# Performance work log

Hardware: AMD Instinct MI355X
Metric: run time of the kernel (lower is better)

The kernel has to match this reference:

```python
import jax, jax.numpy as jnp
import numpy as np

B, T, C = 2, 2048, 1024
H = 16
HS = C // H
EPS = 1e-5


def layernorm(x, g, b):
    mu = jnp.mean(x, axis=-1, keepdims=True)
    var = jnp.var(x, axis=-1, keepdims=True)
    return (x - mu) * jax.lax.rsqrt(var + EPS) * g + b


def setup_inputs() -> dict:
    key = jax.random.key(0)
    ks = jax.random.split(key, 12)
    s_in = 1.0 / np.sqrt(C)
    s_ff = 1.0 / np.sqrt(4 * C)
    return {
        "x": jax.random.normal(ks[0], (B, T, C), jnp.float32),
        "Wq": jax.random.normal(ks[1], (H, C, HS), jnp.float32) * s_in,
        "Wk": jax.random.normal(ks[2], (H, C, HS), jnp.float32) * s_in,
        "Wv": jax.random.normal(ks[3], (H, C, HS), jnp.float32) * s_in,
        "Wo": jax.random.normal(ks[4], (C, C), jnp.float32) * s_in,
        "bo": jnp.zeros((C,), jnp.float32),
        "W1": jax.random.normal(ks[5], (C, 4 * C), jnp.float32) * s_in,
        "b1": jnp.zeros((4 * C,), jnp.float32),
        "W2": jax.random.normal(ks[6], (4 * C, C), jnp.float32) * s_ff,
        "b2": jnp.zeros((C,), jnp.float32),
        "g1": jnp.ones((C,), jnp.float32),
        "be1": jnp.zeros((C,), jnp.float32),
        "g2": jnp.ones((C,), jnp.float32),
        "be2": jnp.zeros((C,), jnp.float32),
    }


def reference(x, Wq, Wk, Wv, Wo, bo, W1, b1, W2, b2, g1, be1, g2, be2):
    # x: [B,T,C]. Dropout is identity (eval mode).
    x = layernorm(x, g1, be1)
    # --- multi-head causal self-attention (per-source: scale by C**-0.5, NOT head_size) ---
    q = jnp.einsum("btc,hcd->bhtd", x, Wq)
    k = jnp.einsum("btc,hcd->bhtd", x, Wk)
    v = jnp.einsum("btc,hcd->bhtd", x, Wv)
    scores = jnp.einsum("bhtd,bhsd->bhts", q, k) * (C ** -0.5)  # [B,H,T,T]
    causal = jnp.tril(jnp.ones((T, T), bool))
    scores = jnp.where(causal, scores, -jnp.inf)
    wei = jax.nn.softmax(scores, axis=-1)
    attn = jnp.einsum("bhts,bhsd->bhtd", wei, v)
    attn = attn.transpose(0, 2, 1, 3).reshape(B, T, C)  # concat heads on last dim
    sa = attn @ Wo + bo
    x = x + sa
    # --- MLP with second pre-op LayerNorm ---
    x = layernorm(x, g2, be2)
    h = jax.nn.relu(x @ W1 + b1)
    x = x + (h @ W2 + b2)
    return x
```

## Files before the change

### kernel.cpp

```cpp
#include <hip/hip_runtime.h>
#include <hip/hip_bf16.h>
#include <math.h>

#define B_ 2
#define T_ 2048
#define C_ 1024
#define H_ 16
#define HS_ 64
#define N_ROWS (B_*T_)
#define MB (1024*1024)

typedef __attribute__((ext_vector_type(8))) short bf16x8;
typedef __attribute__((ext_vector_type(8))) unsigned short u16x8;
typedef __attribute__((ext_vector_type(4))) float floatx4;

static __device__ __forceinline__ unsigned short f2bf(float f) {
  union { float f; unsigned u; } v; v.f = f;
  unsigned r = v.u + 0x7fff + ((v.u >> 16) & 1);
  return (unsigned short)(r >> 16);
}
static __device__ __forceinline__ float bf2f(unsigned short s) {
  union { unsigned u; float f; } v; v.u = ((unsigned)s) << 16;
  return v.f;
}

__global__ __launch_bounds__(256) void ln_kernel(
    const float* __restrict__ x, const float* __restrict__ g,
    const float* __restrict__ b, unsigned short* __restrict__ outb)
{
  const int row = blockIdx.x;
  const int tid = threadIdx.x;
  const float* xr = x + (size_t)row * C_;
  float4 xv = *reinterpret_cast<const float4*>(xr + tid * 4);
  float s  = xv.x + xv.y + xv.z + xv.w;
  float ss = xv.x*xv.x + xv.y*xv.y + xv.z*xv.z + xv.w*xv.w;
  #pragma unroll
  for (int off = 32; off > 0; off >>= 1) {
    s  += __shfl_down(s, off, 64);
    ss += __shfl_down(ss, off, 64);
  }
  __shared__ float rs[4], rss[4];
  __shared__ float smu, srstd;
  if ((tid & 63) == 0) { rs[tid >> 6] = s; rss[tid >> 6] = ss; }
  __syncthreads();
  if (tid == 0) {
    float S  = rs[0] + rs[1] + rs[2] + rs[3];
    float SS = rss[0] + rss[1] + rss[2] + rss[3];
    float mu  = S * (1.0f / C_);
    float var = SS * (1.0f / C_) - mu * mu;
    smu = mu; srstd = rsqrtf(var + 1e-5f);
  }
  __syncthreads();
  const float mu = smu, rstd = srstd;
  float4 gv = *reinterpret_cast<const float4*>(g + tid * 4);
  float4 bv = *reinterpret_cast<const float4*>(b + tid * 4);
  union { unsigned long long ll; unsigned short s[4]; } o;
  o.s[0] = f2bf((xv.x - mu) * rstd * gv.x + bv.x);
  o.s[1] = f2bf((xv.y - mu) * rstd * gv.y + bv.y);
  o.s[2] = f2bf((xv.z - mu) * rstd * gv.z + bv.z);
  o.s[3] = f2bf((xv.w - mu) * rstd * gv.w + bv.w);
  *reinterpret_cast<unsigned long long*>(outb + (size_t)row * C_ + tid * 4) = o.ll;
}

__global__ __launch_bounds__(256) void transpose_cast(
    const float* __restrict__ in, unsigned short* __restrict__ out, int R, int Cc)
{
  __shared__ float tile[32][33];
  const int bz = blockIdx.z;
  in  += (size_t)bz * R * Cc;
  out += (size_t)bz * R * Cc;
  const int tx = threadIdx.x & 31;
  const int ty = threadIdx.x >> 5;
  const int c0 = blockIdx.x * 32, r0 = blockIdx.y * 32;
  #pragma unroll
  for (int j = 0; j < 4; ++j)
    tile[ty + j*8][tx] = in[(size_t)(r0 + ty + j*8) * Cc + c0 + tx];
  __syncthreads();
  #pragma unroll
  for (int j = 0; j < 4; ++j)
    out[(size_t)(c0 + ty + j*8) * R + r0 + tx] = f2bf(tile[tx][ty + j*8]);
}

__global__ __launch_bounds__(256) void transpose_cast_qkv(
    const float* __restrict__ Wq, const float* __restrict__ Wk,
    const float* __restrict__ Wv, unsigned short* __restrict__ out)
{
  __shared__ float tile[32][33];
  const int z = blockIdx.z;
  const int which = z >> 4, h = z & 15;
  const float* in = (which == 0 ? Wq : which == 1 ? Wk : Wv) + (size_t)h * C_ * HS_;
  unsigned short* dst = out + (size_t)z * C_ * HS_;
  const int tx = threadIdx.x & 31;
  const int ty = threadIdx.x >> 5;
  const int c0 = blockIdx.x * 32, r0 = blockIdx.y * 32;
  #pragma unroll
  for (int j = 0; j < 4; ++j)
    tile[ty + j*8][tx] = in[(size_t)(r0 + ty + j*8) * HS_ + c0 + tx];
  __syncthreads();
  #pragma unroll
  for (int j = 0; j < 4; ++j)
    dst[(size_t)(c0 + ty + j*8) * C_ + r0 + tx] = f2bf(tile[tx][ty + j*8]);
}

template<bool RELU, bool HASB>
__global__ __launch_bounds__(512, 2) void gemm256(
    const unsigned short* __restrict__ A,
    const unsigned short* __restrict__ Bt,
    const float* __restrict__ bias,
    unsigned short* __restrict__ Cout,
    int M, int N, int Kfull, int Kh)
{
  __shared__ __align__(16) unsigned short Asl[4 * 8192];
  __shared__ __align__(16) unsigned short Bsl[4 * 8192];
  const int tid = threadIdx.x;
  const int w = tid >> 6, l = tid & 63;
  const int wm = w & 1, wn = w >> 1;
  const int fr = l & 15, fq = l >> 4;
  const int m0 = blockIdx.x * 256, n0 = blockIdx.y * 256;
  const int z = blockIdx.z;

  const unsigned short* Aw = A  + (size_t)m0 * Kfull + (size_t)z * Kh;
  const unsigned short* Bw = Bt + (size_t)n0 * Kfull + (size_t)z * Kh;
  unsigned short* Cw = Cout + (size_t)z * M * N;

  const int g    = ((l & 3) - ((l >> 3) & 3)) & 3;
  const int srow = w * 16 + (l >> 2);
  const unsigned short* ga0 = Aw + (size_t)srow * Kfull + g * 8;
  const unsigned short* ga1 = ga0 + (size_t)128 * Kfull;
  const unsigned short* gb0 = Bw + (size_t)srow * Kfull + g * 8;
  const unsigned short* gb1 = gb0 + (size_t)128 * Kfull;
  unsigned short* da0 = Asl + w * 512;
  unsigned short* db0 = Bsl + w * 512;

  const int Qmax = (Kh >> 5) - 1;

  auto SA = [&](int q) {
    unsigned short* d = da0 + (q & 3) * 8192;
    __builtin_amdgcn_global_load_lds(
        (const __attribute__((address_space(1))) void*)(ga0 + q * 32),
        (__attribute__((address_space(3))) void*)d, 16, 0, 0);
    __builtin_amdgcn_global_load_lds(
        (const __attribute__((address_space(1))) void*)(ga1 + q * 32),
        (__attribute__((address_space(3))) void*)(d + 4096), 16, 0, 0);
  };
  auto SB = [&](int q) {
    unsigned short* d = db0 + (q & 3) * 8192;
    __builtin_amdgcn_global_load_lds(
        (const __attribute__((address_space(1))) void*)(gb0 + q * 32),
        (__attribute__((address_space(3))) void*)d, 16, 0, 0);
    __builtin_amdgcn_global_load_lds(
        (const __attribute__((address_space(1))) void*)(gb1 + q * 32),
        (__attribute__((address_space(3))) void*)(d + 4096), 16, 0, 0);
  };

  const int slot8 = ((fq + (fr >> 1)) & 3) * 8;
  const int aoff = (wm * 128 + fr) * 32 + slot8;
  const int boff = (wn * 64  + fr) * 32 + slot8;

  floatx4 acc[8][4] = {};

  SA(0); SB(0);
  if (Qmax >= 1) { SA(1); SB(1); }
  if (Qmax >= 2) { SA(2); SB(2); }
  asm volatile("s_waitcnt vmcnt(8)" ::: "memory");
  __builtin_amdgcn_s_barrier();

  #pragma unroll 1
  for (int q = 0; q <= Qmax; ++q) {
    const unsigned short* Ar = Asl + (q & 3) * 8192;
    const unsigned short* Br = Bsl + (q & 3) * 8192;
    const bool st = (q + 3 <= Qmax);

    bf16x8 af[4], bfr[4];
    #pragma unroll
    for (int mf = 0; mf < 4; ++mf)
      af[mf] = *(const bf16x8*)(Ar + aoff + mf * 512);
    #pragma unroll
    for (int nf = 0; nf < 4; ++nf)
      bfr[nf] = *(const bf16x8*)(Br + boff + nf * 512);
    if (st) SA(q + 3);
    __builtin_amdgcn_s_barrier();
    asm volatile("s_waitcnt lgkmcnt(0)" ::: "memory");
    __builtin_amdgcn_s_setprio(1);
    #pragma unroll
    for (int mf = 0; mf < 4; ++mf)
      #pragma unroll
      for (int nf = 0; nf < 4; ++nf)
        acc[mf][nf] = __builtin_amdgcn_mfma_f32_16x16x32_bf16(
            af[mf], bfr[nf], acc[mf][nf], 0, 0, 0);
    __builtin_amdgcn_s_setprio(0);
    __builtin_amdgcn_s_barrier();

    bf16x8 af2[4];
    #pragma unroll
    for (int mf = 0; mf < 4; ++mf)
      af2[mf] = *(const bf16x8*)(Ar + aoff + (4 + mf) * 512);
    if (st) SB(q + 3);
    if (q + 3 <= Qmax)        { asm volatile("s_waitcnt vmcnt(8)" ::: "memory"); }
    else if (q + 2 == Qmax)   { asm volatile("s_waitcnt vmcnt(4)" ::: "memory"); }
    else if (q + 1 == Qmax)   { asm volatile("s_waitcnt vmcnt(0)" ::: "memory"); }
    __builtin_amdgcn_s_barrier();
    asm volatile("s_waitcnt lgkmcnt(0)" ::: "memory");
    __builtin_amdgcn_s_setprio(1);
    #pragma unroll
    for (int mf = 0; mf < 4; ++mf)
      #pragma unroll
      for (int nf = 0; nf < 4; ++nf)
        acc[4 + mf][nf] = __builtin_amdgcn_mfma_f32_16x16x32_bf16(
            af2[mf], bfr[nf], acc[4 + mf][nf], 0, 0, 0);
    __builtin_amdgcn_s_setprio(0);
    __builtin_amdgcn_s_barrier();
  }

  #pragma unroll
  for (int nf = 0; nf < 4; ++nf) {
    const int col = n0 + wn * 64 + nf * 16 + fr;
    const float bv = HASB ? bias[col] : 0.0f;
    #pragma unroll
    for (int mf = 0; mf < 8; ++mf) {
      #pragma unroll
      for (int r = 0; r < 4; ++r) {
        const int row = m0 + wm * 128 + mf * 16 + fq * 4 + r;
        float v = acc[mf][nf][r] + bv;
        if (RELU) v = v > 0.0f ? v : 0.0f;
        Cw[(size_t)row * N + col] = f2bf(v);
      }
    }
  }
}

template<int TNB, bool OUTBF16, bool RELU, bool HASB, bool HASRES>
__global__ __launch_bounds__(256) void gemm_bf16(
    const unsigned short* __restrict__ A,
    const unsigned short* __restrict__ Bt,
    const float* __restrict__ bias,
    const unsigned short* __restrict__ res,
    void* __restrict__ Cout,
    int M, int N, int K)
{
  constexpr int NT = TNB / 32;
  constexpr int WN = TNB / 2;
  constexpr int LOADS = 4 + 2 * (TNB / 64);
  __shared__ unsigned short As[2][2][128 * 32];
  __shared__ unsigned short Bs[2][2][TNB * 32];
  const int tid  = threadIdx.x;
  const int lane = tid & 63;
  const int wave = tid >> 6;
  const int wm = wave & 1, wn = wave >> 1;
  const int m0 = blockIdx.x * 128, n0 = blockIdx.y * TNB;

  const int lrow = lane >> 2;
  const int lcol = (lane & 3) * 8;
  const int fr = lane & 15;
  const int fq = lane >> 4;

  floatx4 acc[4][NT] = {};

  const unsigned short* Aw = A  + (size_t)m0 * K;
  const unsigned short* Bw = Bt + (size_t)n0 * K;

  auto STAGE = [&](int bb, int k0) {
    #pragma unroll
    for (int half = 0; half < 2; ++half) {
      #pragma unroll
      for (int i = 0; i < 2; ++i) {
        const int rbase = i * 64 + wave * 16;
        const unsigned short* gp =
            Aw + (size_t)(rbase + lrow) * K + k0 + half * 32 + lcol;
        __builtin_amdgcn_global_load_lds(
            (const __attribute__((address_space(1))) void*)gp,
            (__attribute__((address_space(3))) void*)(As[bb][half] + rbase * 32),
            16, 0, 0);
      }
      #pragma unroll
      for (int i = 0; i < TNB / 64; ++i) {
        const int rbase = i * 64 + wave * 16;
        const unsigned short* gp =
            Bw + (size_t)(rbase + lrow) * K + k0 + half * 32 + lcol;
        __builtin_amdgcn_global_load_lds(
            (const __attribute__((address_space(1))) void*)gp,
            (__attribute__((address_space(3))) void*)(Bs[bb][half] + rbase * 32),
            16, 0, 0);
      }
    }
  };

  auto COMPUTE = [&](int bb) {
    #pragma unroll
    for (int half = 0; half < 2; ++half) {
      bf16x8 af[4], bfr[NT];
      #pragma unroll
      for (int t = 0; t < 4; ++t)
        af[t]  = *reinterpret_cast<const bf16x8*>(
            As[bb][half] + (wm*64 + t*16 + fr)*32 + fq*8);
      #pragma unroll
      for (int t = 0; t < NT; ++t)
        bfr[t] = *reinterpret_cast<const bf16x8*>(
            Bs[bb][half] + (wn*WN + t*16 + fr)*32 + fq*8);
      #pragma unroll
      for (int mt = 0; mt < 4; ++mt)
        #pragma unroll
        for (int nt = 0; nt < NT; ++nt)
          acc[mt][nt] = __builtin_amdgcn_mfma_f32_16x16x32_bf16(
              af[mt], bfr[nt], acc[mt][nt], 0, 0, 0);
    }
  };

  STAGE(0, 0);
  int bb = 0;
  for (int k0 = 64; k0 < K; k0 += 64) {
    STAGE(bb ^ 1, k0);
    asm volatile("s_waitcnt vmcnt(%0)" :: "n"(LOADS) : "memory");
    __builtin_amdgcn_s_barrier();
    COMPUTE(bb);
    __builtin_amdgcn_s_barrier();
    bb ^= 1;
  }
  asm volatile("s_waitcnt vmcnt(0)" ::: "memory");
  __builtin_amdgcn_s_barrier();
  COMPUTE(bb);

  #pragma unroll
  for (int nt = 0; nt < NT; ++nt) {
    const int col = n0 + wn*WN + nt*16 + fr;
    const float bv = HASB ? bias[col] : 0.0f;
    #pragma unroll
    for (int mt = 0; mt < 4; ++mt) {
      #pragma unroll
      for (int r = 0; r < 4; ++r) {
        const int row = m0 + wm*64 + mt*16 + fq*4 + r;
        float v = acc[mt][nt][r] + bv;
        if (RELU) v = v > 0.0f ? v : 0.0f;
        if (HASRES) v += bf2f(res[(size_t)row * N + col]);
        if (OUTBF16) ((unsigned short*)Cout)[(size_t)row * N + col] = f2bf(v);
        else         ((float*)Cout)[(size_t)row * N + col] = v;
      }
    }
  }
}

template<int SPLITS>
__global__ __launch_bounds__(256) void splitk_reduce(
    const unsigned short* __restrict__ p,
    const float* __restrict__ bias, const unsigned short* __restrict__ res,
    float* __restrict__ out)
{
  const size_t i = ((size_t)blockIdx.x * 256 + threadIdx.x) * 4;
  const size_t MN = (size_t)N_ROWS * C_;
  float4 bv = *reinterpret_cast<const float4*>(bias + (i & (size_t)(C_ - 1)));
  float acc[4] = {bv.x, bv.y, bv.z, bv.w};
  {
    const unsigned short* rp = res + i;
    #pragma unroll
    for (int j = 0; j < 4; ++j) acc[j] += bf2f(rp[j]);
  }
  #pragma unroll
  for (int z = 0; z < SPLITS; ++z) {
    const unsigned short* pp = p + (size_t)z * MN + i;
    #pragma unroll
    for (int j = 0; j < 4; ++j) acc[j] += bf2f(pp[j]);
  }
  float4 o; o.x = acc[0]; o.y = acc[1]; o.z = acc[2]; o.w = acc[3];
  *reinterpret_cast<float4*>(out + i) = o;
}

__global__ __launch_bounds__(256) void v_transpose(
    const unsigned short* __restrict__ qkv, unsigned short* __restrict__ vt)
{
  __shared__ __align__(16) unsigned short sT[64][72];
  const int st = blockIdx.x;
  const int bh = blockIdx.y;
  const int b = bh >> 4, h = bh & 15;
  const int t = threadIdx.x;
  const int r = t >> 2, c0 = (t & 3) * 16;
  const unsigned short* src =
      qkv + (size_t)(b * T_ + st * 64 + r) * 3072 + 2048 + h * 64 + c0;
  *(u16x8*)&sT[r][c0]     = *(const u16x8*)src;
  *(u16x8*)&sT[r][c0 + 8] = *(const u16x8*)(src + 8);
  __syncthreads();
  const int d = t >> 2, sc = (t & 3) * 16;
  unsigned short v[16];
  #pragma unroll
  for (int j = 0; j < 16; ++j) v[j] = sT[sc + j][d];
  unsigned short* dst = vt + ((size_t)bh * 64 + d) * (size_t)T_ + st * 64 + sc;
  *(uint4*)dst       = *(uint4*)&v[0];
  *(uint4*)(dst + 8) = *(uint4*)&v[8];
}

__global__ __launch_bounds__(256, 3) void attn_mfma(
    const unsigned short* __restrict__ qkv,
    const unsigned short* __restrict__ vt,
    unsigned short* __restrict__ out)
{
  const int bh = blockIdx.x;
  const int qt = (int)(gridDim.y - 1) - (int)blockIdx.y;
  const int b = bh >> 4, h = bh & 15;
  const int tid = threadIdx.x;
  const int w = tid >> 6;
  const int lane = tid & 63;
  const int l15 = lane & 15, fq = lane >> 4;
  const int t0 = qt * 64;
  const int q_row = t0 + w * 16 + l15;

  __shared__ __align__(16) unsigned short sK [128][72];
  __shared__ __align__(16) unsigned short sVt[64][136];
  __shared__ __align__(16) unsigned short sP [64][136];

  const float c1 = 1.4426950408889634f / 32.0f;

  bf16x8 aq[2];
  {
    const unsigned short* qp = qkv + (size_t)(b*T_ + q_row)*3072 + h*HS_ + fq*8;
    aq[0] = *(const bf16x8*)qp;
    aq[1] = *(const bf16x8*)(qp + 32);
  }

  const int nks = (qt >> 1) + 1;

  const int kr = tid >> 1, kc = (tid & 1) * 32;
  const int vr = tid >> 2, vc = (tid & 3) * 32;
  const unsigned short* kp0 =
      qkv + (size_t)(b*T_ + kr)*3072 + C_ + h*HS_ + kc;
  const unsigned short* vp0 =
      vt + ((size_t)bh*64 + vr)*(size_t)T_ + vc;

  u16x8 kg0, kg1, kg2, kg3, vg0, vg1, vg2, vg3;
  kg0 = *(const u16x8*)kp0;      kg1 = *(const u16x8*)(kp0 + 8);
  kg2 = *(const u16x8*)(kp0+16); kg3 = *(const u16x8*)(kp0 + 24);
  vg0 = *(const u16x8*)vp0;      vg1 = *(const u16x8*)(vp0 + 8);
  vg2 = *(const u16x8*)(vp0+16); vg3 = *(const u16x8*)(vp0 + 24);
  *(u16x8*)&sK [kr][kc]      = kg0; *(u16x8*)&sK [kr][kc + 8]  = kg1;
  *(u16x8*)&sK [kr][kc + 16] = kg2; *(u16x8*)&sK [kr][kc + 24] = kg3;
  *(u16x8*)&sVt[vr][vc]      = vg0; *(u16x8*)&sVt[vr][vc + 8]  = vg1;
  *(u16x8*)&sVt[vr][vc + 16] = vg2; *(u16x8*)&sVt[vr][vc + 24] = vg3;

  floatx4 oacc[4] = {};
  float m_s = -3.0e38f, l_s = 0.0f;

  #pragma unroll 1
  for (int ks = 0; ks < nks; ++ks) {
    asm volatile("s_waitcnt lgkmcnt(0)" ::: "memory");
    __builtin_amdgcn_s_barrier();

    if (ks + 1 < nks) {
      const unsigned short* kp = kp0 + (size_t)(ks + 1) * (128 * 3072);
      kg0 = *(const u16x8*)kp;        kg1 = *(const u16x8*)(kp + 8);
      kg2 = *(const u16x8*)(kp + 16); kg3 = *(const u16x8*)(kp + 24);
      const unsigned short* vp = vp0 + (ks + 1) * 128;
      vg0 = *(const u16x8*)vp;        vg1 = *(const u16x8*)(vp + 8);
      vg2 = *(const u16x8*)(vp + 16); vg3 = *(const u16x8*)(vp + 24);
    }

    floatx4 stacc[8] = {};
    __builtin_amdgcn_s_setprio(1);
    #pragma unroll
    for (int st = 0; st < 8; ++st) {
      bf16x8 ka = *(const bf16x8*)&sK[st*16 + l15][fq*8];
      bf16x8 kb = *(const bf16x8*)&sK[st*16 + l15][32 + fq*8];
      stacc[st] = __builtin_amdgcn_mfma_f32_16x16x32_bf16(ka, aq[0], stacc[st], 0, 0, 0);
      stacc[st] = __builtin_amdgcn_mfma_f32_16x16x32_bf16(kb, aq[1], stacc[st], 0, 0, 0);
    }
    __builtin_amdgcn_s_setprio(0);

    if (ks == nks - 1) {
      const int sbase = ks*128 + fq*4;
      #pragma unroll
      for (int st = 0; st < 8; ++st)
        #pragma unroll
        for (int r = 0; r < 4; ++r)
          if (sbase + st*16 + r > q_row) stacc[st][r] = -3.0e38f;
    }

    float mx = -3.0e38f;
    #pragma unroll
    for (int st = 0; st < 8; ++st)
      #pragma unroll
      for (int r = 0; r < 4; ++r) mx = fmaxf(mx, stacc[st][r]);
    mx = fmaxf(mx, __shfl_xor(mx, 16, 64));
    mx = fmaxf(mx, __shfl_xor(mx, 32, 64));

    float mnew;
    if (__all((mx - m_s) * c1 <= 8.0f)) {
      mnew = m_s;
    } else {
      mnew = fmaxf(m_s, mx);
      const float alpha = __builtin_amdgcn_exp2f((m_s - mnew) * c1);
      #pragma unroll
      for (int r = 0; r < 4; ++r) {
        const float ar = __shfl(alpha, fq*4 + r, 64);
        #pragma unroll
        for (int dt = 0; dt < 4; ++dt) oacc[dt][r] *= ar;
      }
      l_s *= alpha;
      m_s = mnew;
    }

    const float mc = mnew * c1;
    float sum = 0.0f;
    #pragma unroll
    for (int st = 0; st < 8; ++st) {
      unsigned pu[4];
      #pragma unroll
      for (int r = 0; r < 4; ++r) {
        const float p = __builtin_amdgcn_exp2f(stacc[st][r] * c1 - mc);
        sum += p;
        union { float f; unsigned u; } cv; cv.f = p;
        pu[r] = cv.u + 0x8000u;
      }
      const unsigned lo = __builtin_amdgcn_perm(pu[1], pu[0], 0x07060302u);
      const unsigned hi = __builtin_amdgcn_perm(pu[3], pu[2], 0x07060302u);
      *(unsigned long long*)&sP[w*16 + l15][st*16 + fq*4] =
          ((unsigned long long)hi << 32) | lo;
    }
    sum += __shfl_xor(sum, 16, 64);
    sum += __shfl_xor(sum, 32, 64);
    l_s += sum;

    __builtin_amdgcn_s_setprio(1);
    #pragma unroll
    for (int c = 0; c < 4; ++c) {
      bf16x8 ap = *(const bf16x8*)&sP[w*16 + l15][c*32 + fq*8];
      #pragma unroll
      for (int dt = 0; dt < 4; ++dt) {
        bf16x8 bv = *(const bf16x8*)&sVt[dt*16 + l15][c*32 + fq*8];
        oacc[dt] = __builtin_amdgcn_mfma_f32_16x16x32_bf16(ap, bv, oacc[dt], 0, 0, 0);
      }
    }
    __builtin_amdgcn_s_setprio(0);

    asm volatile("s_waitcnt lgkmcnt(0)" ::: "memory");
    __builtin_amdgcn_s_barrier();
    if (ks + 1 < nks) {
      *(u16x8*)&sK [kr][kc]      = kg0; *(u16x8*)&sK [kr][kc + 8]  = kg1;
      *(u16x8*)&sK [kr][kc + 16] = kg2; *(u16x8*)&sK [kr][kc + 24] = kg3;
      *(u16x8*)&sVt[vr][vc]      = vg0; *(u16x8*)&sVt[vr][vc + 8]  = vg1;
      *(u16x8*)&sVt[vr][vc + 16] = vg2; *(u16x8*)&sVt[vr][vc + 24] = vg3;
    }
  }

  #pragma unroll
  for (int r = 0; r < 4; ++r) {
    const float il = 1.0f / __shfl(l_s, fq*4 + r, 64);
    const int q = t0 + w*16 + fq*4 + r;
    #pragma unroll
    for (int dt = 0; dt < 4; ++dt)
      out[(size_t)(b*T_ + q)*C_ + h*HS_ + dt*16 + l15] = f2bf(oacc[dt][r] * il);
  }
}

extern "C" void kernel_launch(void* const* d_in, const int* in_sizes, int n_in,
                              void* d_out, int out_size, void* d_ws, size_t ws_size,
                              hipStream_t stream)
{
  const float* x   = (const float*)d_in[0];
  const float* Wq  = (const float*)d_in[1];
  const float* Wk  = (const float*)d_in[2];
  const float* Wv  = (const float*)d_in[3];
  const float* Wo  = (const float*)d_in[4];
  const float* bo  = (const float*)d_in[5];
  const float* W1  = (const float*)d_in[6];
  const float* b1  = (const float*)d_in[7];
  const float* W2  = (const float*)d_in[8];
  const float* b2  = (const float*)d_in[9];
  const float* g1  = (const float*)d_in[10];
  const float* be1 = (const float*)d_in[11];
  const float* g2  = (const float*)d_in[12];
  const float* be2 = (const float*)d_in[13];
  float* out = (float*)d_out;

  char* ws = (char*)d_ws;
  unsigned short* BtQKV = (unsigned short*)(ws + (size_t) 0*MB);
  unsigned short* BtWo  = (unsigned short*)(ws + (size_t) 6*MB);
  unsigned short* BtW1  = (unsigned short*)(ws + (size_t) 8*MB);
  unsigned short* BtW2  = (unsigned short*)(ws + (size_t)16*MB);
  unsigned short* lnb   = (unsigned short*)(ws + (size_t)24*MB);
  unsigned short* qkvb  = (unsigned short*)(ws + (size_t)32*MB);
  unsigned short* vtb   = (unsigned short*)(ws + (size_t)56*MB);
  unsigned short* attnb = (unsigned short*)(ws + (size_t)64*MB);
  float*          x2    = (float*)         (ws + (size_t)32*MB);
  unsigned short* hb    = (unsigned short*)(ws + (size_t)32*MB);
  unsigned short* pk4   = (unsigned short*)(ws + (size_t)64*MB);

  dim3 blk(256);
  dim3 blk512(512);

  transpose_cast_qkv<<<dim3(HS_/32, C_/32, 3*H_), blk, 0, stream>>>(Wq, Wk, Wv, BtQKV);
  transpose_cast<<<dim3(C_/32,  C_/32, 1),  blk, 0, stream>>>(Wo, BtWo, C_, C_);
  transpose_cast<<<dim3(4*C_/32,C_/32, 1),  blk, 0, stream>>>(W1, BtW1, C_, 4*C_);
  transpose_cast<<<dim3(C_/32,4*C_/32, 1),  blk, 0, stream>>>(W2, BtW2, 4*C_, C_);

  ln_kernel<<<dim3(N_ROWS), blk, 0, stream>>>(x, g1, be1, lnb);

  gemm256<false,false><<<dim3(N_ROWS/256, 3072/256, 1), blk512, 0, stream>>>(
      lnb, BtQKV, nullptr, qkvb, N_ROWS, 3072, C_, C_);

  v_transpose<<<dim3(T_/64, B_*H_), blk, 0, stream>>>(qkvb, vtb);

  attn_mfma<<<dim3(B_*H_, T_/64), blk, 0, stream>>>(qkvb, vtb, attnb);

  gemm_bf16<64,false,false,true,true><<<dim3(N_ROWS/128, C_/64), blk, 0, stream>>>(
      attnb, BtWo, bo, lnb, x2, N_ROWS, C_, C_);

  ln_kernel<<<dim3(N_ROWS), blk, 0, stream>>>(x2, g2, be2, lnb);

  gemm256<true,true><<<dim3(N_ROWS/256, 4*C_/256, 1), blk512, 0, stream>>>(
      lnb, BtW1, b1, hb, N_ROWS, 4*C_, C_, C_);

  gemm256<false,false><<<dim3(N_ROWS/256, C_/256, 4), blk512, 0, stream>>>(
      hb, BtW2, nullptr, pk4, N_ROWS, C_, 4*C_, C_);

  splitk_reduce<4><<<dim3((N_ROWS * C_) / (256 * 4)), blk, 0, stream>>>(
      pk4, b2, lnb, out);
}
```

Before: 342.9 us.

## Double-buffer GEMM LDS fragments and prefetch next k-step during MFMA

The GEMM main loop is restructured into a two-step unrolled HALF lambda. The next k-step's A and B fragments are read from LDS into a second register set (bfA/bfB ping-pong) while the second batch of MFMAs for the current step runs. Explicit lgkmcnt waits are dropped, and sched_barriers pin the instruction order. The aim is to hide LDS read latency behind matrix math, at the cost of more vector registers. The loop now assumes Qmax is odd.

```diff
diff --git a/kernel.cpp b/kernel.cpp
--- a/kernel.cpp
+++ b/kernel.cpp
@@ -158,58 +158,66 @@
   const int boff = (wn * 64  + fr) * 32 + slot8;
 
   floatx4 acc[8][4] = {};
+  bf16x8 af[4], af2[4], bfA[4], bfB[4];
 
   SA(0); SB(0);
   if (Qmax >= 1) { SA(1); SB(1); }
   if (Qmax >= 2) { SA(2); SB(2); }
   asm volatile("s_waitcnt vmcnt(8)" ::: "memory");
   __builtin_amdgcn_s_barrier();
-
-  #pragma unroll 1
-  for (int q = 0; q <= Qmax; ++q) {
-    const unsigned short* Ar = Asl + (q & 3) * 8192;
-    const unsigned short* Br = Bsl + (q & 3) * 8192;
-    const bool st = (q + 3 <= Qmax);
-
-    bf16x8 af[4], bfr[4];
+  #pragma unroll
+  for (int mf = 0; mf < 4; ++mf) af[mf]  = *(const bf16x8*)(Asl + aoff + mf * 512);
+  #pragma unroll
+  for (int nf = 0; nf < 4; ++nf) bfA[nf] = *(const bf16x8*)(Bsl + boff + nf * 512);
+
+  auto HALF = [&](int h, bf16x8 (&bfC)[4], bf16x8 (&bfN)[4]) {
+    const unsigned short* Ar = Asl + (h & 3) * 8192;
     #pragma unroll
     for (int mf = 0; mf < 4; ++mf)
-      af[mf] = *(const bf16x8*)(Ar + aoff + mf * 512);
-    #pragma unroll
-    for (int nf = 0; nf < 4; ++nf)
-      bfr[nf] = *(const bf16x8*)(Br + boff + nf * 512);
-    if (st) SA(q + 3);
-    __builtin_amdgcn_s_barrier();
-    asm volatile("s_waitcnt lgkmcnt(0)" ::: "memory");
+      af2[mf] = *(const bf16x8*)(Ar + aoff + (4 + mf) * 512);
+    if (h + 3 <= Qmax) SA(h + 3);
+    __builtin_amdgcn_sched_barrier(0);
+    __builtin_amdgcn_s_barrier();
     __builtin_amdgcn_s_setprio(1);
     #pragma unroll
     for (int mf = 0; mf < 4; ++mf)
       #pragma unroll
       for (int nf = 0; nf < 4; ++nf)
         acc[mf][nf] = __builtin_amdgcn_mfma_f32_16x16x32_bf16(
-            af[mf], bfr[nf], acc[mf][nf], 0, 0, 0);
+            af[mf], bfC[nf], acc[mf][nf], 0, 0, 0);
     __builtin_amdgcn_s_setprio(0);
     __builtin_amdgcn_s_barrier();
-
-    bf16x8 af2[4];
-    #pragma unroll
-    for (int mf = 0; mf < 4; ++mf)
-      af2[mf] = *(const bf16x8*)(Ar + aoff + (4 + mf) * 512);
-    if (st) SB(q + 3);
-    if (q + 3 <= Qmax)        { asm volatile("s_waitcnt vmcnt(8)" ::: "memory"); }
-    else if (q + 2 == Qmax)   { asm volatile("s_waitcnt vmcnt(4)" ::: "memory"); }
-    else if (q + 1 == Qmax)   { asm volatile("s_waitcnt vmcnt(0)" ::: "memory"); }
-    __builtin_amdgcn_s_barrier();
-    asm volatile("s_waitcnt lgkmcnt(0)" ::: "memory");
+    if (h + 3 <= Qmax) SB(h + 3);
+    if (h + 3 <= Qmax)        { asm volatile("s_waitcnt vmcnt(8)" ::: "memory"); }
+    else if (h + 2 == Qmax)   { asm volatile("s_waitcnt vmcnt(4)" ::: "memory"); }
+    else if (h + 1 == Qmax)   { asm volatile("s_waitcnt vmcnt(0)" ::: "memory"); }
+    __builtin_amdgcn_s_barrier();
+    if (h < Qmax) {
+      const unsigned short* Ar2 = Asl + ((h + 1) & 3) * 8192;
+      const unsigned short* Br2 = Bsl + ((h + 1) & 3) * 8192;
+      #pragma unroll
+      for (int mf = 0; mf < 4; ++mf)
+        af[mf] = *(const bf16x8*)(Ar2 + aoff + mf * 512);
+      #pragma unroll
+      for (int nf = 0; nf < 4; ++nf)
+        bfN[nf] = *(const bf16x8*)(Br2 + boff + nf * 512);
+    }
+    __builtin_amdgcn_sched_barrier(0);
     __builtin_amdgcn_s_setprio(1);
     #pragma unroll
     for (int mf = 0; mf < 4; ++mf)
       #pragma unroll
       for (int nf = 0; nf < 4; ++nf)
         acc[4 + mf][nf] = __builtin_amdgcn_mfma_f32_16x16x32_bf16(
-            af2[mf], bfr[nf], acc[4 + mf][nf], 0, 0, 0);
+            af2[mf], bfC[nf], acc[4 + mf][nf], 0, 0, 0);
     __builtin_amdgcn_s_setprio(0);
     __builtin_amdgcn_s_barrier();
+  };
+
+  #pragma unroll 1
+  for (int q = 0; q < Qmax; q += 2) {
+    HALF(q,     bfA, bfB);
+    HALF(q + 1, bfB, bfA);
   }
 
   #pragma unroll
```

Measured after the change: 350.7 us. 1.02x slower.

## Shrink gemm256 tile to 128x256 with double-buffered LDS pipeline

Applied to the files above, without the earlier changes.

Shrinks the large GEMM kernel's M tile from 256 to 128 rows and replaces the 4-stage, split-phase LDS pipeline with a simple 2-stage double buffer. The occupancy hint rises to 4 blocks per CU. Smaller LDS and register footprints plus twice as many blocks aim to improve occupancy and load balance. The cost is less data reuse per block, more global traffic for B, and a shallower prefetch that waits on vmcnt(0) every iteration, so memory latency may be exposed.

```diff
diff --git a/kernel.cpp b/kernel.cpp
--- a/kernel.cpp
+++ b/kernel.cpp
@@ -103,20 +103,20 @@
 }
 
 template<bool RELU, bool HASB>
-__global__ __launch_bounds__(512, 2) void gemm256(
+__global__ __launch_bounds__(512, 4) void gemm256(
     const unsigned short* __restrict__ A,
     const unsigned short* __restrict__ Bt,
     const float* __restrict__ bias,
     unsigned short* __restrict__ Cout,
     int M, int N, int Kfull, int Kh)
 {
-  __shared__ __align__(16) unsigned short Asl[4 * 8192];
-  __shared__ __align__(16) unsigned short Bsl[4 * 8192];
+  __shared__ __align__(16) unsigned short Asl[2 * 4096];
+  __shared__ __align__(16) unsigned short Bsl[2 * 8192];
   const int tid = threadIdx.x;
   const int w = tid >> 6, l = tid & 63;
   const int wm = w & 1, wn = w >> 1;
   const int fr = l & 15, fq = l >> 4;
-  const int m0 = blockIdx.x * 256, n0 = blockIdx.y * 256;
+  const int m0 = blockIdx.x * 128, n0 = blockIdx.y * 256;
   const int z = blockIdx.z;
 
   const unsigned short* Aw = A  + (size_t)m0 * Kfull + (size_t)z * Kh;
@@ -125,8 +125,7 @@
 
   const int g    = ((l & 3) - ((l >> 3) & 3)) & 3;
   const int srow = w * 16 + (l >> 2);
-  const unsigned short* ga0 = Aw + (size_t)srow * Kfull + g * 8;
-  const unsigned short* ga1 = ga0 + (size_t)128 * Kfull;
+  const unsigned short* ga  = Aw + (size_t)srow * Kfull + g * 8;
   const unsigned short* gb0 = Bw + (size_t)srow * Kfull + g * 8;
   const unsigned short* gb1 = gb0 + (size_t)128 * Kfull;
   unsigned short* da0 = Asl + w * 512;
@@ -134,53 +133,42 @@
 
   const int Qmax = (Kh >> 5) - 1;
 
-  auto SA = [&](int q) {
-    unsigned short* d = da0 + (q & 3) * 8192;
+  auto STAGE = [&](int q) {
+    unsigned short* da = da0 + (q & 1) * 4096;
+    unsigned short* db = db0 + (q & 1) * 8192;
     __builtin_amdgcn_global_load_lds(
-        (const __attribute__((address_space(1))) void*)(ga0 + q * 32),
-        (__attribute__((address_space(3))) void*)d, 16, 0, 0);
-    __builtin_amdgcn_global_load_lds(
-        (const __attribute__((address_space(1))) void*)(ga1 + q * 32),
-        (__attribute__((address_space(3))) void*)(d + 4096), 16, 0, 0);
-  };
-  auto SB = [&](int q) {
-    unsigned short* d = db0 + (q & 3) * 8192;
+        (const __attribute__((address_space(1))) void*)(ga + q * 32),
+        (__attribute__((address_space(3))) void*)da, 16, 0, 0);
     __builtin_amdgcn_global_load_lds(
         (const __attribute__((address_space(1))) void*)(gb0 + q * 32),
-        (__attribute__((address_space(3))) void*)d, 16, 0, 0);
+        (__attribute__((address_space(3))) void*)db, 16, 0, 0);
     __builtin_amdgcn_global_load_lds(
         (const __attribute__((address_space(1))) void*)(gb1 + q * 32),
-        (__attribute__((address_space(3))) void*)(d + 4096), 16, 0, 0);
+        (__attribute__((address_space(3))) void*)(db + 4096), 16, 0, 0);
   };
 
   const int slot8 = ((fq + (fr >> 1)) & 3) * 8;
-  const int aoff = (wm * 128 + fr) * 32 + slot8;
-  const int boff = (wn * 64  + fr) * 32 + slot8;
-
-  floatx4 acc[8][4] = {};
-
-  SA(0); SB(0);
-  if (Qmax >= 1) { SA(1); SB(1); }
-  if (Qmax >= 2) { SA(2); SB(2); }
-  asm volatile("s_waitcnt vmcnt(8)" ::: "memory");
+  const int aoff = (wm * 64 + fr) * 32 + slot8;
+  const int boff = (wn * 64 + fr) * 32 + slot8;
+
+  floatx4 acc[4][4] = {};
+
+  STAGE(0);
+  asm volatile("s_waitcnt vmcnt(0)" ::: "memory");
   __builtin_amdgcn_s_barrier();
 
   #pragma unroll 1
   for (int q = 0; q <= Qmax; ++q) {
-    const unsigned short* Ar = Asl + (q & 3) * 8192;
-    const unsigned short* Br = Bsl + (q & 3) * 8192;
-    const bool st = (q + 3 <= Qmax);
-
+    if (q < Qmax) STAGE(q + 1);
+    const unsigned short* Ar = Asl + (q & 1) * 4096;
+    const unsigned short* Br = Bsl + (q & 1) * 8192;
     bf16x8 af[4], bfr[4];
     #pragma unroll
     for (int mf = 0; mf < 4; ++mf)
-      af[mf] = *(const bf16x8*)(Ar + aoff + mf * 512);
+      af[mf]  = *(const bf16x8*)(Ar + aoff + mf * 512);
     #pragma unroll
     for (int nf = 0; nf < 4; ++nf)
       bfr[nf] = *(const bf16x8*)(Br + boff + nf * 512);
-    if (st) SA(q + 3);
-    __builtin_amdgcn_s_barrier();
-    asm volatile("s_waitcnt lgkmcnt(0)" ::: "memory");
     __builtin_amdgcn_s_setprio(1);
     #pragma unroll
     for (int mf = 0; mf < 4; ++mf)
@@ -189,26 +177,7 @@
         acc[mf][nf] = __builtin_amdgcn_mfma_f32_16x16x32_bf16(
             af[mf], bfr[nf], acc[mf][nf], 0, 0, 0);
     __builtin_amdgcn_s_setprio(0);
-    __builtin_amdgcn_s_barrier();
-
-    bf16x8 af2[4];
-    #pragma unroll
-    for (int mf = 0; mf < 4; ++mf)
-      af2[mf] = *(const bf16x8*)(Ar + aoff + (4 + mf) * 512);
-    if (st) SB(q + 3);
-    if (q + 3 <= Qmax)        { asm volatile("s_waitcnt vmcnt(8)" ::: "memory"); }
-    else if (q + 2 == Qmax)   { asm volatile("s_waitcnt vmcnt(4)" ::: "memory"); }
-    else if (q + 1 == Qmax)   { asm volatile("s_waitcnt vmcnt(0)" ::: "memory"); }
-    __builtin_amdgcn_s_barrier();
-    asm volatile("s_waitcnt lgkmcnt(0)" ::: "memory");
-    __builtin_amdgcn_s_setprio(1);
-    #pragma unroll
-    for (int mf = 0; mf < 4; ++mf)
-      #pragma unroll
-      for (int nf = 0; nf < 4; ++nf)
-        acc[4 + mf][nf] = __builtin_amdgcn_mfma_f32_16x16x32_bf16(
-            af2[mf], bfr[nf], acc[4 + mf][nf], 0, 0, 0);
-    __builtin_amdgcn_s_setprio(0);
+    if (q < Qmax) { asm volatile("s_waitcnt vmcnt(0)" ::: "memory"); }
     __builtin_amdgcn_s_barrier();
   }
 
@@ -217,10 +186,10 @@
     const int col = n0 + wn * 64 + nf * 16 + fr;
     const float bv = HASB ? bias[col] : 0.0f;
     #pragma unroll
-    for (int mf = 0; mf < 8; ++mf) {
+    for (int mf = 0; mf < 4; ++mf) {
       #pragma unroll
       for (int r = 0; r < 4; ++r) {
-        const int row = m0 + wm * 128 + mf * 16 + fq * 4 + r;
+        const int row = m0 + wm * 64 + mf * 16 + fq * 4 + r;
         float v = acc[mf][nf][r] + bv;
         if (RELU) v = v > 0.0f ? v : 0.0f;
         Cw[(size_t)row * N + col] = f2bf(v);
@@ -591,7 +560,7 @@
 
   ln_kernel<<<dim3(N_ROWS), blk, 0, stream>>>(x, g1, be1, lnb);
 
-  gemm256<false,false><<<dim3(N_ROWS/256, 3072/256, 1), blk512, 0, stream>>>(
+  gemm256<false,false><<<dim3(N_ROWS/128, 3072/256, 1), blk512, 0, stream>>>(
       lnb, BtQKV, nullptr, qkvb, N_ROWS, 3072, C_, C_);
 
   v_transpose<<<dim3(T_/64, B_*H_), blk, 0, stream>>>(qkvb, vtb);
@@ -603,10 +572,10 @@
 
   ln_kernel<<<dim3(N_ROWS), blk, 0, stream>>>(x2, g2, be2, lnb);
 
-  gemm256<true,true><<<dim3(N_ROWS/256, 4*C_/256, 1), blk512, 0, stream>>>(
+  gemm256<true,true><<<dim3(N_ROWS/128, 4*C_/256, 1), blk512, 0, stream>>>(
       lnb, BtW1, b1, hb, N_ROWS, 4*C_, C_, C_);
 
-  gemm256<false,false><<<dim3(N_ROWS/256, C_/256, 4), blk512, 0, stream>>>(
+  gemm256<false,false><<<dim3(N_ROWS/128, C_/256, 4), blk512, 0, stream>>>(
       hb, BtW2, nullptr, pk4, N_ROWS, C_, 4*C_, C_);
 
   splitk_reduce<4><<<dim3((N_ROWS * C_) / (256 * 4)), blk, 0, stream>>>(
```

After: 332.7 us. 3.0% less time.
